# Optimization experiments

Measured on AMD Instinct MI355X. Metric: run time of the kernel, lower is better.

## Reference

```python
import jax, jax.numpy as jnp
import numpy as np

B, CH, CW, H, FH, FW = 32, 16, 16, 8, 4, 4
NQ = 64
NK = CH * FH * CW * FW  # 4096
D_IN, D_V, D_MODEL = 512, 64, 512


def setup_inputs() -> dict:
    key = jax.random.key(0)
    k1, k2, k3, k4, k5 = jax.random.split(key, 5)
    att12 = jax.random.uniform(k1, (B, CH, CW, H, FH, FW), dtype=jnp.float32)
    att3 = jax.random.uniform(k2, (B, H, NQ, CH * CW), dtype=jnp.float32)
    values = jax.random.normal(k3, (B, NK, D_IN), dtype=jnp.float32)
    # Learned params (xavier-ish scale)
    W_v = jax.random.normal(k4, (H * D_V, D_IN), dtype=jnp.float32) * (1.0 / np.sqrt(D_IN))
    b_v = jnp.zeros((H * D_V,), dtype=jnp.float32)
    W_o = jax.random.normal(k5, (D_MODEL, H * D_V), dtype=jnp.float32) * (1.0 / np.sqrt(H * D_V))
    b_o = jnp.zeros((D_MODEL,), dtype=jnp.float32)
    return {"att12": att12, "att3": att3, "values": values,
            "W_v": W_v, "b_v": b_v, "W_o": W_o, "b_o": b_o}


def reference(att12, att3, values, W_v, b_v, W_o, b_o):
    b_s, h, nq, _ = att3.shape
    ch = cw = CH
    fh, fw = att12.shape[-2:]
    nk = values.shape[1]
    d_v = W_v.shape[0] // h
    # v: [b, h, nk, d_v]
    v = (values @ W_v.T + b_v).reshape(b_s, nk, h, d_v).transpose(0, 2, 1, 3)
    # att12 -> [b, h, 1, ch, cw, fh, fw]
    a12 = jnp.transpose(att12, (0, 3, 1, 2, 4, 5))[:, :, None]
    # att3 -> [b, h, nq, ch, cw, 1, 1]
    a3 = att3.reshape(b_s, h, nq, ch, cw, 1, 1)
    # broadcast multiply, then interleave to key order (ch, fh, cw, fw)
    att = (a12 * a3).transpose(0, 1, 2, 3, 5, 4, 6).reshape(b_s, h, nq, nk)
    att = jax.nn.softmax(att, axis=-1)
    out = jnp.einsum('bhqk,bhkd->bhqd', att, v)
    out = out.transpose(0, 2, 1, 3).reshape(b_s, nq, h * d_v)
    return out @ W_o.T + b_o
```

## Files before the change

kernel.cpp:

```cpp
#include <hip/hip_runtime.h>
#include <stdint.h>

#define BB 32
#define HH 8
#define NQ 64
#define NK 4096
#define DIN 512
#define DV 64
#define DM 512

typedef short bf16x8 __attribute__((ext_vector_type(8)));
typedef short bf16x4 __attribute__((ext_vector_type(4)));
typedef float f32x4 __attribute__((ext_vector_type(4)));

__device__ __forceinline__ unsigned short f2bf(float f) {
  union { float f; unsigned u; } v; v.f = f;
  unsigned r = v.u + 0x7fffu + ((v.u >> 16) & 1u);
  return (unsigned short)(r >> 16);
}

__device__ __forceinline__ void gld_lds16(const void* g, void* l) {
  __builtin_amdgcn_global_load_lds(
      (const __attribute__((address_space(1))) void*)g,
      (__attribute__((address_space(3))) void*)l, 16, 0, 0);
}

__global__ __launch_bounds__(256) void convf2bf(const float* __restrict__ in,
                                                unsigned short* __restrict__ out) {
  long i = (long)(blockIdx.x * 256 + threadIdx.x) * 4;
  f32x4 d = *(const f32x4*)(in + i);
  bf16x4 o;
  o[0] = (short)f2bf(d[0]); o[1] = (short)f2bf(d[1]);
  o[2] = (short)f2bf(d[2]); o[3] = (short)f2bf(d[3]);
  *(bf16x4*)(out + i) = o;
}

__global__ __launch_bounds__(64) void zsum_kernel(const float* __restrict__ att12,
                                                  const float* __restrict__ att3,
                                                  float* __restrict__ rZ) {
  const int bhq = blockIdx.x;
  const int h = (bhq >> 6) & 7;
  const int b = bhq >> 9;
  const int l = threadIdx.x;
  const int ch = l >> 2, fh = l & 3;
  const float* a3p = att3 + (long)bhq * 256 + ch * 16;
  const float* a12p = att12 + (long)(b * 16 + ch) * 2048 + h * 16 + fh * 4;
  float sum = 0.f;
#pragma unroll
  for (int cw = 0; cw < 16; ++cw) {
    float y = a3p[cw];
    f32x4 x = *(const f32x4*)(a12p + cw * 128);
#pragma unroll
    for (int fw = 0; fw < 4; ++fw) sum += __expf(x[fw] * y);
  }
#pragma unroll
  for (int off = 32; off > 0; off >>= 1) sum += __shfl_down(sum, off);
  if (l == 0) rZ[bhq] = 1.0f / sum;
}

__global__ __launch_bounds__(256) void transpose_conv(const float* __restrict__ V,
                                                      unsigned short* __restrict__ Vt) {
  int id = blockIdx.x;
  int kt = id & 63;
  int ct = (id >> 6) & 7;
  int b = id >> 9;
  const int t = threadIdx.x;
  __shared__ __align__(16) unsigned short T[64][72];

  const float* vp = V + (long)b * (4096L * 512) + (long)(kt * 64) * 512 + ct * 64;
  int cc = (t & 15) * 4;
  int kk0 = t >> 4;
#pragma unroll
  for (int r = 0; r < 4; ++r) {
    int kk = kk0 + r * 16;
    f32x4 d = *(const f32x4*)(vp + (long)kk * 512 + cc);
    T[cc + 0][kk] = f2bf(d[0]);
    T[cc + 1][kk] = f2bf(d[1]);
    T[cc + 2][kk] = f2bf(d[2]);
    T[cc + 3][kk] = f2bf(d[3]);
  }
  __syncthreads();
  unsigned short* op = Vt + (long)b * (512L * 4096) + (long)(ct * 64) * 4096 + (long)(kt * 64);
#pragma unroll
  for (int s = 0; s < 2; ++s) {
    int li = s * 256 + t;
    int c = li >> 3, k8 = (li & 7) * 8;
    bf16x8 d = *(const bf16x8*)(&T[c][k8]);
    *(bf16x8*)(op + (long)c * 4096 + k8) = d;
  }
}

__global__ __launch_bounds__(256, 2) void fused_u_gemm(
    const float* __restrict__ att12, const float* __restrict__ att3,
    const float* __restrict__ rZ, const unsigned short* __restrict__ Vt,
    unsigned short* __restrict__ U) {
  const int id = blockIdx.x;
  const int xcd = id & 7, rest = id >> 3;
  const int m_t = rest & 3, bh = rest >> 2;
  const int b = bh * 2 + (xcd & 1);
  const int n_t = xcd >> 1;
  const int m0 = m_t * 128, n0 = n_t * 128;
  const int t = threadIdx.x, lane = t & 63, wave = t >> 6;

  const unsigned short* Vb = Vt + (long)b * (512L * 4096) + (long)n0 * 4096;
  __shared__ __align__(16) unsigned short As[128 * 32];
  __shared__ __align__(16) unsigned short Bs[128 * 32];

  const int r = t >> 1;
  const int kh = (t & 1) * 16;
  const int m = m0 + r, h = m >> 6, q = m & 63;
  const float* a3row = att3 + ((long)(b * 8 + h) * 64 + q) * 256;
  const float* a12bh = att12 + (long)b * 32768 + h * 16;

  const int wm = (wave >> 1) * 64, wn = (wave & 1) * 64;
  const int l16 = lane & 15, quad = lane >> 4;

  f32x4 acc[4][4];
#pragma unroll
  for (int i = 0; i < 4; ++i)
#pragma unroll
    for (int j = 0; j < 4; ++j) acc[i][j] = (f32x4){0.f, 0.f, 0.f, 0.f};

  for (int k0 = 0; k0 < 4096; k0 += 32) {
    {
      int row = t >> 2, kq = (t & 3) * 8;
      gld_lds16(Vb + (long)row * 4096 + k0 + kq, (char*)Bs + (wave * 64) * 16);
      int li = 256 + t;
      row = li >> 2; kq = (li & 3) * 8;
      gld_lds16(Vb + (long)row * 4096 + k0 + kq, (char*)Bs + (256 + wave * 64) * 16);
    }
    {
      int k = k0 + kh;
      int ch = k >> 8, fh = (k >> 6) & 3, cw0 = (k >> 2) & 15;
      f32x4 y = *(const f32x4*)(a3row + ch * 16 + cw0);
      const float* a12p = a12bh + (long)ch * 2048 + cw0 * 128 + fh * 4;
      bf16x8 p0, p1;
#pragma unroll
      for (int c4 = 0; c4 < 2; ++c4) {
        f32x4 x = *(const f32x4*)(a12p + c4 * 128);
#pragma unroll
        for (int fw = 0; fw < 4; ++fw) p0[c4 * 4 + fw] = (short)f2bf(__expf(x[fw] * y[c4]));
      }
#pragma unroll
      for (int c4 = 2; c4 < 4; ++c4) {
        f32x4 x = *(const f32x4*)(a12p + c4 * 128);
#pragma unroll
        for (int fw = 0; fw < 4; ++fw) p1[(c4 - 2) * 4 + fw] = (short)f2bf(__expf(x[fw] * y[c4]));
      }
      *(bf16x8*)(As + r * 32 + kh) = p0;
      *(bf16x8*)(As + r * 32 + kh + 8) = p1;
    }
    __syncthreads();
    bf16x8 af[4], bfr[4];
#pragma unroll
    for (int i = 0; i < 4; ++i)
      af[i] = *(const bf16x8*)(As + (wm + i * 16 + l16) * 32 + quad * 8);
#pragma unroll
    for (int j = 0; j < 4; ++j)
      bfr[j] = *(const bf16x8*)(Bs + (wn + j * 16 + l16) * 32 + quad * 8);
#pragma unroll
    for (int i = 0; i < 4; ++i)
#pragma unroll
      for (int j = 0; j < 4; ++j)
        acc[i][j] = __builtin_amdgcn_mfma_f32_16x16x32_bf16(af[i], bfr[j], acc[i][j], 0, 0, 0);
    __syncthreads();
  }

  const float* rzb = rZ + (long)b * 512;
  unsigned short* Ub = U + (long)b * 262144;
#pragma unroll
  for (int i = 0; i < 4; ++i) {
#pragma unroll
    for (int j = 0; j < 4; ++j) {
      int col = n0 + wn + j * 16 + l16;
#pragma unroll
      for (int rr = 0; rr < 4; ++rr) {
        int row = m0 + wm + i * 16 + quad * 4 + rr;
        float v = acc[i][j][rr] * rzb[row];
        Ub[(long)row * 512 + col] = f2bf(v);
      }
    }
  }
}

template <int BM, int BN, bool OUT_BF16, bool ADD_BIAS>
__global__ __launch_bounds__(256, 2) void gemm_bt(
    const unsigned short* __restrict__ A, const unsigned short* __restrict__ Bt,
    void* __restrict__ C, const float* __restrict__ bias,
    int K, int lda, int ldb, int ldc,
    long sA, long sB, int zmodB,
    long sC1, long sC2, int zdivC,
    long sBias, int zmodBias) {
  constexpr int BK = 32;
  const int t = threadIdx.x;
  const int lane = t & 63;
  const int wave = t >> 6;
  const int z = blockIdx.z;
  const int m0 = blockIdx.y * BM;
  const int n0 = blockIdx.x * BN;

  A += (long)z * sA + (long)m0 * lda;
  Bt += (long)(z % zmodB) * sB + (long)n0 * ldb;

  __shared__ __align__(16) unsigned short As[BM * BK];
  __shared__ __align__(16) unsigned short Bs[BN * BK];

  constexpr int TM = BM / 32;
  constexpr int TN = BN / 32;
  const int wm = (wave >> 1) * (BM / 2);
  const int wn = (wave & 1) * (BN / 2);
  const int l16 = lane & 15;
  const int quad = lane >> 4;

  f32x4 acc[TM][TN];
#pragma unroll
  for (int i = 0; i < TM; ++i)
#pragma unroll
    for (int j = 0; j < TN; ++j) acc[i][j] = (f32x4){0.f, 0.f, 0.f, 0.f};

  constexpr int ASHOT = (BM * 4) / 256;
  constexpr int BSHOT = (BN * 4) / 256;

  for (int k0 = 0; k0 < K; k0 += BK) {
#pragma unroll
    for (int s = 0; s < ASHOT; ++s) {
      int li = s * 256 + t;
      int row = li >> 2, kq = (li & 3) * 8;
      gld_lds16(A + (long)row * lda + k0 + kq, (char*)As + (s * 256 + wave * 64) * 16);
    }
#pragma unroll
    for (int s = 0; s < BSHOT; ++s) {
      int li = s * 256 + t;
      int row = li >> 2, kq = (li & 3) * 8;
      gld_lds16(Bt + (long)row * ldb + k0 + kq, (char*)Bs + (s * 256 + wave * 64) * 16);
    }
    __syncthreads();
    bf16x8 af[TM], bfr[TN];
#pragma unroll
    for (int i = 0; i < TM; ++i)
      af[i] = *(const bf16x8*)(As + (wm + i * 16 + l16) * BK + quad * 8);
#pragma unroll
    for (int j = 0; j < TN; ++j)
      bfr[j] = *(const bf16x8*)(Bs + (wn + j * 16 + l16) * BK + quad * 8);
#pragma unroll
    for (int i = 0; i < TM; ++i)
#pragma unroll
      for (int j = 0; j < TN; ++j)
        acc[i][j] = __builtin_amdgcn_mfma_f32_16x16x32_bf16(af[i], bfr[j], acc[i][j], 0, 0, 0);
    __syncthreads();
  }

  long coff = (long)(z / zdivC) * sC1 + (long)(z % zdivC) * sC2;
  const float* bp = nullptr;
  if (ADD_BIAS) bp = bias + (long)(z % zmodBias) * sBias + n0;
#pragma unroll
  for (int i = 0; i < TM; ++i) {
#pragma unroll
    for (int j = 0; j < TN; ++j) {
      int col = wn + j * 16 + l16;
#pragma unroll
      for (int r = 0; r < 4; ++r) {
        int row = wm + i * 16 + quad * 4 + r;
        float v = acc[i][j][r];
        if (ADD_BIAS) v += bp[col];
        long idx = coff + (long)(m0 + row) * ldc + (n0 + col);
        if (OUT_BF16) ((unsigned short*)C)[idx] = f2bf(v);
        else ((float*)C)[idx] = v;
      }
    }
  }
}

extern "C" void kernel_launch(void* const* d_in, const int* in_sizes, int n_in,
                              void* d_out, int out_size, void* d_ws, size_t ws_size,
                              hipStream_t stream) {
  const float* att12 = (const float*)d_in[0];
  const float* att3  = (const float*)d_in[1];
  const float* values = (const float*)d_in[2];
  const float* W_v = (const float*)d_in[3];
  const float* b_v = (const float*)d_in[4];
  const float* W_o = (const float*)d_in[5];
  const float* b_o = (const float*)d_in[6];
  float* out = (float*)d_out;

  char* ws = (char*)d_ws;
  unsigned short* Vt  = (unsigned short*)(ws);
  unsigned short* U   = (unsigned short*)(ws + 134217728L);
  unsigned short* Vo  = (unsigned short*)(ws + 150994944L);
  unsigned short* Wvb = (unsigned short*)(ws + 153092096L);
  unsigned short* Wob = (unsigned short*)(ws + 153616384L);
  float*          rZ  = (float*)(ws + 154140672L);

  convf2bf<<<dim3(256), dim3(256), 0, stream>>>(W_v, Wvb);
  convf2bf<<<dim3(256), dim3(256), 0, stream>>>(W_o, Wob);
  zsum_kernel<<<dim3(16384), dim3(64), 0, stream>>>(att12, att3, rZ);
  transpose_conv<<<dim3(16384), dim3(256), 0, stream>>>(values, Vt);

  fused_u_gemm<<<dim3(512), dim3(256), 0, stream>>>(att12, att3, rZ, Vt, U);

  gemm_bt<64, 64, true, true><<<dim3(1, 1, 256), dim3(256), 0, stream>>>(
      U, Wvb, Vo, b_v, 512, 512, 512, 512,
      32768L, 32768L, 8,
      32768L, 64L, 8,
      64L, 8);

  gemm_bt<128, 128, false, true><<<dim3(4, 16, 1), dim3(256), 0, stream>>>(
      Vo, Wob, out, b_o, 512, 512, 512, 512,
      0L, 0L, 1,
      0L, 0L, 1,
      0L, 1);

  (void)in_sizes; (void)n_in; (void)out_size; (void)ws_size;
}
```

Measured before the change: 608.7 us.

## Reorder computation: project values per head first, then attention, fuse softmax sum

Projects the values through W_v first, computing vT = W_v·V^T per batch with on-the-fly fp32→bf16 conversion. This replaces the separate transpose/convert pass and the old U=P·V GEMM over 512 input channels with a per-head P·v GEMM over 64 channels. The softmax denominator is now accumulated inside the attention GEMM across two K-splits, which removes the standalone zsum pass. Normalisation and b_v are applied while loading the output-projection operand, and the two K-split partials are summed through a duplicated W_o. The cost is more GEMM FLOPs in the projection, an fp32 intermediate, and a cross-wave LDS reduction.

After: 635.6 us. +4.4%, slower.

```diff
diff --git a/kernel.cpp b/kernel.cpp
--- a/kernel.cpp
+++ b/kernel.cpp
@@ -1,13 +1,4 @@
 #include <hip/hip_runtime.h>
-#include <stdint.h>
-
-#define BB 32
-#define HH 8
-#define NQ 64
-#define NK 4096
-#define DIN 512
-#define DV 64
-#define DM 512
 
 typedef short bf16x8 __attribute__((ext_vector_type(8)));
 typedef short bf16x4 __attribute__((ext_vector_type(4)));
@@ -25,8 +16,8 @@
       (__attribute__((address_space(3))) void*)l, 16, 0, 0);
 }
 
-__global__ __launch_bounds__(256) void convf2bf(const float* __restrict__ in,
-                                                unsigned short* __restrict__ out) {
+__global__ __launch_bounds__(256) void convWv(const float* __restrict__ in,
+                                              unsigned short* __restrict__ out) {
   long i = (long)(blockIdx.x * 256 + threadIdx.x) * 4;
   f32x4 d = *(const f32x4*)(in + i);
   bf16x4 o;
@@ -35,85 +26,33 @@
   *(bf16x4*)(out + i) = o;
 }
 
-__global__ __launch_bounds__(64) void zsum_kernel(const float* __restrict__ att12,
-                                                  const float* __restrict__ att3,
-                                                  float* __restrict__ rZ) {
-  const int bhq = blockIdx.x;
-  const int h = (bhq >> 6) & 7;
-  const int b = bhq >> 9;
-  const int l = threadIdx.x;
-  const int ch = l >> 2, fh = l & 3;
-  const float* a3p = att3 + (long)bhq * 256 + ch * 16;
-  const float* a12p = att12 + (long)(b * 16 + ch) * 2048 + h * 16 + fh * 4;
-  float sum = 0.f;
-#pragma unroll
-  for (int cw = 0; cw < 16; ++cw) {
-    float y = a3p[cw];
-    f32x4 x = *(const f32x4*)(a12p + cw * 128);
-#pragma unroll
-    for (int fw = 0; fw < 4; ++fw) sum += __expf(x[fw] * y);
-  }
-#pragma unroll
-  for (int off = 32; off > 0; off >>= 1) sum += __shfl_down(sum, off);
-  if (l == 0) rZ[bhq] = 1.0f / sum;
-}
-
-__global__ __launch_bounds__(256) void transpose_conv(const float* __restrict__ V,
-                                                      unsigned short* __restrict__ Vt) {
-  int id = blockIdx.x;
-  int kt = id & 63;
-  int ct = (id >> 6) & 7;
-  int b = id >> 9;
-  const int t = threadIdx.x;
-  __shared__ __align__(16) unsigned short T[64][72];
-
-  const float* vp = V + (long)b * (4096L * 512) + (long)(kt * 64) * 512 + ct * 64;
-  int cc = (t & 15) * 4;
-  int kk0 = t >> 4;
-#pragma unroll
-  for (int r = 0; r < 4; ++r) {
-    int kk = kk0 + r * 16;
-    f32x4 d = *(const f32x4*)(vp + (long)kk * 512 + cc);
-    T[cc + 0][kk] = f2bf(d[0]);
-    T[cc + 1][kk] = f2bf(d[1]);
-    T[cc + 2][kk] = f2bf(d[2]);
-    T[cc + 3][kk] = f2bf(d[3]);
-  }
-  __syncthreads();
-  unsigned short* op = Vt + (long)b * (512L * 4096) + (long)(ct * 64) * 4096 + (long)(kt * 64);
-#pragma unroll
-  for (int s = 0; s < 2; ++s) {
-    int li = s * 256 + t;
-    int c = li >> 3, k8 = (li & 7) * 8;
-    bf16x8 d = *(const bf16x8*)(&T[c][k8]);
-    *(bf16x8*)(op + (long)c * 4096 + k8) = d;
-  }
-}
-
-__global__ __launch_bounds__(256, 2) void fused_u_gemm(
-    const float* __restrict__ att12, const float* __restrict__ att3,
-    const float* __restrict__ rZ, const unsigned short* __restrict__ Vt,
-    unsigned short* __restrict__ U) {
-  const int id = blockIdx.x;
-  const int xcd = id & 7, rest = id >> 3;
-  const int m_t = rest & 3, bh = rest >> 2;
-  const int b = bh * 2 + (xcd & 1);
-  const int n_t = xcd >> 1;
-  const int m0 = m_t * 128, n0 = n_t * 128;
+__global__ __launch_bounds__(256) void convWo2(const float* __restrict__ in,
+                                               unsigned short* __restrict__ out) {
+  long i4 = (long)(blockIdx.x * 256 + threadIdx.x) * 4;
+  int e = (int)(i4 >> 9), c = (int)(i4 & 511);
+  f32x4 d = *(const f32x4*)(in + i4);
+  bf16x4 o;
+  o[0] = (short)f2bf(d[0]); o[1] = (short)f2bf(d[1]);
+  o[2] = (short)f2bf(d[2]); o[3] = (short)f2bf(d[3]);
+  *(bf16x4*)(out + (long)e * 1024 + c) = o;
+  *(bf16x4*)(out + (long)e * 1024 + 512 + c) = o;
+}
+
+__global__ __launch_bounds__(256, 2) void vt_gemm(
+    const unsigned short* __restrict__ Wvb, const float* __restrict__ V,
+    unsigned short* __restrict__ vT) {
   const int t = threadIdx.x, lane = t & 63, wave = t >> 6;
-
-  const unsigned short* Vb = Vt + (long)b * (512L * 4096) + (long)n0 * 4096;
-  __shared__ __align__(16) unsigned short As[128 * 32];
-  __shared__ __align__(16) unsigned short Bs[128 * 32];
-
-  const int r = t >> 1;
-  const int kh = (t & 1) * 16;
-  const int m = m0 + r, h = m >> 6, q = m & 63;
-  const float* a3row = att3 + ((long)(b * 8 + h) * 64 + q) * 256;
-  const float* a12bh = att12 + (long)b * 32768 + h * 16;
+  const int n0 = blockIdx.x * 128;
+  const int m0 = blockIdx.y * 128;
+  const int b = blockIdx.z;
+  const float* Vb = V + (long)b * (4096L * 512) + (long)n0 * 512;
+
+  __shared__ __align__(16) unsigned short As[128 * 64];
+  __shared__ __align__(16) unsigned short Bs[128 * 64];
 
   const int wm = (wave >> 1) * 64, wn = (wave & 1) * 64;
   const int l16 = lane & 15, quad = lane >> 4;
+  const int bchunk = (t & 15) * 4, brow0 = t >> 4;
 
   f32x4 acc[4][4];
 #pragma unroll
@@ -121,154 +60,236 @@
 #pragma unroll
     for (int j = 0; j < 4; ++j) acc[i][j] = (f32x4){0.f, 0.f, 0.f, 0.f};
 
-  for (int k0 = 0; k0 < 4096; k0 += 32) {
-    {
-      int row = t >> 2, kq = (t & 3) * 8;
-      gld_lds16(Vb + (long)row * 4096 + k0 + kq, (char*)Bs + (wave * 64) * 16);
-      int li = 256 + t;
-      row = li >> 2; kq = (li & 3) * 8;
-      gld_lds16(Vb + (long)row * 4096 + k0 + kq, (char*)Bs + (256 + wave * 64) * 16);
-    }
-    {
-      int k = k0 + kh;
-      int ch = k >> 8, fh = (k >> 6) & 3, cw0 = (k >> 2) & 15;
-      f32x4 y = *(const f32x4*)(a3row + ch * 16 + cw0);
-      const float* a12p = a12bh + (long)ch * 2048 + cw0 * 128 + fh * 4;
-      bf16x8 p0, p1;
-#pragma unroll
-      for (int c4 = 0; c4 < 2; ++c4) {
-        f32x4 x = *(const f32x4*)(a12p + c4 * 128);
-#pragma unroll
-        for (int fw = 0; fw < 4; ++fw) p0[c4 * 4 + fw] = (short)f2bf(__expf(x[fw] * y[c4]));
-      }
-#pragma unroll
-      for (int c4 = 2; c4 < 4; ++c4) {
-        f32x4 x = *(const f32x4*)(a12p + c4 * 128);
-#pragma unroll
-        for (int fw = 0; fw < 4; ++fw) p1[(c4 - 2) * 4 + fw] = (short)f2bf(__expf(x[fw] * y[c4]));
-      }
-      *(bf16x8*)(As + r * 32 + kh) = p0;
-      *(bf16x8*)(As + r * 32 + kh + 8) = p1;
-    }
-    __syncthreads();
-    bf16x8 af[4], bfr[4];
-#pragma unroll
-    for (int i = 0; i < 4; ++i)
-      af[i] = *(const bf16x8*)(As + (wm + i * 16 + l16) * 32 + quad * 8);
-#pragma unroll
-    for (int j = 0; j < 4; ++j)
-      bfr[j] = *(const bf16x8*)(Bs + (wn + j * 16 + l16) * 32 + quad * 8);
-#pragma unroll
-    for (int i = 0; i < 4; ++i)
+  for (int k0 = 0; k0 < 512; k0 += 64) {
+#pragma unroll
+    for (int s = 0; s < 4; ++s) {
+      int li = s * 256 + t;
+      int row = li >> 3, kq = (li & 7) * 8;
+      gld_lds16(Wvb + (long)(m0 + row) * 512 + k0 + kq, (char*)As + (s * 256 + wave * 64) * 16);
+    }
+#pragma unroll
+    for (int j = 0; j < 8; ++j) {
+      int row = brow0 + 16 * j;
+      f32x4 d = *(const f32x4*)(Vb + (long)row * 512 + k0 + bchunk);
+      bf16x4 p;
+      p[0] = (short)f2bf(d[0]); p[1] = (short)f2bf(d[1]);
+      p[2] = (short)f2bf(d[2]); p[3] = (short)f2bf(d[3]);
+      *(bf16x4*)(Bs + row * 64 + bchunk) = p;
+    }
+    __syncthreads();
+#pragma unroll
+    for (int ks = 0; ks < 2; ++ks) {
+      bf16x8 af[4], bfv[4];
+#pragma unroll
+      for (int i = 0; i < 4; ++i)
+        af[i] = *(const bf16x8*)(As + (wm + i * 16 + l16) * 64 + ks * 32 + quad * 8);
 #pragma unroll
       for (int j = 0; j < 4; ++j)
-        acc[i][j] = __builtin_amdgcn_mfma_f32_16x16x32_bf16(af[i], bfr[j], acc[i][j], 0, 0, 0);
-    __syncthreads();
-  }
-
-  const float* rzb = rZ + (long)b * 512;
-  unsigned short* Ub = U + (long)b * 262144;
-#pragma unroll
-  for (int i = 0; i < 4; ++i) {
+        bfv[j] = *(const bf16x8*)(Bs + (wn + j * 16 + l16) * 64 + ks * 32 + quad * 8);
+#pragma unroll
+      for (int i = 0; i < 4; ++i)
+#pragma unroll
+        for (int j = 0; j < 4; ++j)
+          acc[i][j] = __builtin_amdgcn_mfma_f32_16x16x32_bf16(af[i], bfv[j], acc[i][j], 0, 0, 0);
+    }
+    __syncthreads();
+  }
+  unsigned short* o = vT + (long)b * 2097152;
+#pragma unroll
+  for (int i = 0; i < 4; ++i)
 #pragma unroll
     for (int j = 0; j < 4; ++j) {
       int col = n0 + wn + j * 16 + l16;
 #pragma unroll
-      for (int rr = 0; rr < 4; ++rr) {
-        int row = m0 + wm + i * 16 + quad * 4 + rr;
-        float v = acc[i][j][rr] * rzb[row];
-        Ub[(long)row * 512 + col] = f2bf(v);
+      for (int r = 0; r < 4; ++r) {
+        int row = m0 + wm + i * 16 + quad * 4 + r;
+        o[(long)row * 4096 + col] = f2bf(acc[i][j][r]);
       }
     }
-  }
-}
-
-template <int BM, int BN, bool OUT_BF16, bool ADD_BIAS>
-__global__ __launch_bounds__(256, 2) void gemm_bt(
-    const unsigned short* __restrict__ A, const unsigned short* __restrict__ Bt,
-    void* __restrict__ C, const float* __restrict__ bias,
-    int K, int lda, int ldb, int ldc,
-    long sA, long sB, int zmodB,
-    long sC1, long sC2, int zdivC,
-    long sBias, int zmodBias) {
-  constexpr int BK = 32;
-  const int t = threadIdx.x;
-  const int lane = t & 63;
-  const int wave = t >> 6;
-  const int z = blockIdx.z;
-  const int m0 = blockIdx.y * BM;
-  const int n0 = blockIdx.x * BN;
-
-  A += (long)z * sA + (long)m0 * lda;
-  Bt += (long)(z % zmodB) * sB + (long)n0 * ldb;
-
-  __shared__ __align__(16) unsigned short As[BM * BK];
-  __shared__ __align__(16) unsigned short Bs[BN * BK];
-
-  constexpr int TM = BM / 32;
-  constexpr int TN = BN / 32;
-  const int wm = (wave >> 1) * (BM / 2);
-  const int wn = (wave & 1) * (BN / 2);
-  const int l16 = lane & 15;
-  const int quad = lane >> 4;
-
-  f32x4 acc[TM][TN];
-#pragma unroll
-  for (int i = 0; i < TM; ++i)
-#pragma unroll
-    for (int j = 0; j < TN; ++j) acc[i][j] = (f32x4){0.f, 0.f, 0.f, 0.f};
-
-  constexpr int ASHOT = (BM * 4) / 256;
-  constexpr int BSHOT = (BN * 4) / 256;
-
-  for (int k0 = 0; k0 < K; k0 += BK) {
-#pragma unroll
-    for (int s = 0; s < ASHOT; ++s) {
+}
+
+__global__ __launch_bounds__(256, 2) void o_gemm(
+    const float* __restrict__ att12, const float* __restrict__ att3,
+    const unsigned short* __restrict__ vT, float* __restrict__ O32,
+    float* __restrict__ Zp) {
+  const int bh = blockIdx.x, part = blockIdx.y;
+  const int b = bh >> 3, h = bh & 7;
+  const int t = threadIdx.x, lane = t & 63, wave = t >> 6;
+
+  __shared__ __align__(16) unsigned short As[4 * 64 * 32];
+  __shared__ __align__(16) unsigned short Bs[4 * 64 * 32];
+  __shared__ float Ored[64 * 64];
+  __shared__ float Zl[4][64];
+
+  const unsigned short* vTb = vT + (long)b * 2097152 + (long)h * 64 * 4096;
+  const int gq = t & 63, gw = t >> 6;
+  const float* a3row = att3 + ((long)bh * 64 + gq) * 256;
+  const float* a12b = att12 + (long)b * 32768 + h * 16;
+  const int l16 = lane & 15, quad = lane >> 4;
+  const int kw0 = part * 2048 + gw * 512;
+
+  f32x4 acc[4][4];
+#pragma unroll
+  for (int i = 0; i < 4; ++i)
+#pragma unroll
+    for (int j = 0; j < 4; ++j) acc[i][j] = (f32x4){0.f, 0.f, 0.f, 0.f};
+  float zacc = 0.f;
+
+  for (int it = 0; it < 16; ++it) {
+#pragma unroll
+    for (int s = 0; s < 4; ++s) {
+      int row = t >> 2, kq = (t & 3) * 8;
+      int kk = part * 2048 + s * 512 + it * 32 + kq;
+      gld_lds16(vTb + (long)row * 4096 + kk, (char*)Bs + s * 4096 + wave * 1024);
+    }
+    {
+      int kbase = kw0 + it * 32;
+      int ch = kbase >> 8, fh = (kbase >> 6) & 3, cw0 = (kbase >> 2) & 15;
+      f32x4 y0 = *(const f32x4*)(a3row + ch * 16 + cw0);
+      f32x4 y1 = *(const f32x4*)(a3row + ch * 16 + cw0 + 4);
+      const float* ap = a12b + ch * 2048 + cw0 * 128 + fh * 4;
+      bf16x8 p[4];
+#pragma unroll
+      for (int cw = 0; cw < 8; ++cw) {
+        float y = (cw < 4) ? y0[cw] : y1[cw - 4];
+        f32x4 x = *(const f32x4*)(ap + cw * 128);
+#pragma unroll
+        for (int fw = 0; fw < 4; ++fw) {
+          float e = __expf(x[fw] * y);
+          zacc += e;
+          p[cw >> 1][(cw & 1) * 4 + fw] = (short)f2bf(e);
+        }
+      }
+#pragma unroll
+      for (int g = 0; g < 4; ++g)
+        *(bf16x8*)(As + gw * 2048 + gq * 32 + g * 8) = p[g];
+    }
+    __syncthreads();
+    bf16x8 af[4], bfv[4];
+#pragma unroll
+    for (int i = 0; i < 4; ++i)
+      af[i] = *(const bf16x8*)(As + wave * 2048 + (i * 16 + l16) * 32 + quad * 8);
+#pragma unroll
+    for (int j = 0; j < 4; ++j)
+      bfv[j] = *(const bf16x8*)(Bs + wave * 2048 + (j * 16 + l16) * 32 + quad * 8);
+#pragma unroll
+    for (int i = 0; i < 4; ++i)
+#pragma unroll
+      for (int j = 0; j < 4; ++j)
+        acc[i][j] = __builtin_amdgcn_mfma_f32_16x16x32_bf16(af[i], bfv[j], acc[i][j], 0, 0, 0);
+    __syncthreads();
+  }
+
+  Zl[gw][gq] = zacc;
+#pragma unroll
+  for (int w = 0; w < 4; ++w) {
+    if (wave == w) {
+#pragma unroll
+      for (int i = 0; i < 4; ++i)
+#pragma unroll
+        for (int j = 0; j < 4; ++j) {
+          int col = j * 16 + l16;
+#pragma unroll
+          for (int r = 0; r < 4; ++r) {
+            int row = i * 16 + quad * 4 + r;
+            if (w == 0) Ored[row * 64 + col] = acc[i][j][r];
+            else Ored[row * 64 + col] += acc[i][j][r];
+          }
+        }
+    }
+    __syncthreads();
+  }
+  if (t < 64) {
+    float z = Zl[0][t] + Zl[1][t] + Zl[2][t] + Zl[3][t];
+    Zp[(long)part * 16384 + (long)bh * 64 + t] = z;
+  }
+  {
+    int q = t >> 2, c0 = (t & 3) * 16;
+    float* op = O32 + (long)part * 1048576 + ((long)(b * 64 + q)) * 512 + h * 64 + c0;
+#pragma unroll
+    for (int j = 0; j < 4; ++j)
+      *(f32x4*)(op + j * 4) = *(const f32x4*)(Ored + q * 64 + c0 + j * 4);
+  }
+}
+
+__global__ __launch_bounds__(256) void rzcomb(const float* __restrict__ Zp,
+                                              float* __restrict__ rZ) {
+  int i = blockIdx.x * 256 + threadIdx.x;
+  rZ[i] = 1.0f / (Zp[i] + Zp[16384 + i]);
+}
+
+__global__ __launch_bounds__(256, 2) void wo_gemm(
+    const float* __restrict__ O32, const float* __restrict__ rZ,
+    const float* __restrict__ b_v, const unsigned short* __restrict__ Wo2,
+    const float* __restrict__ b_o, float* __restrict__ out) {
+  const int t = threadIdx.x, lane = t & 63, wave = t >> 6;
+  const int n0 = blockIdx.x * 128;
+  const int m0 = blockIdx.y * 64;
+
+  __shared__ __align__(16) unsigned short As[64 * 32];
+  __shared__ __align__(16) unsigned short Bs[128 * 32];
+
+  const int wm = (wave >> 1) * 32, wn = (wave & 1) * 64;
+  const int l16 = lane & 15, quad = lane >> 4;
+  const int arow = t >> 2, akq = (t & 3) * 8;
+  const int m = m0 + arow, ab = m >> 6, aq = m & 63;
+
+  f32x4 acc[2][4];
+#pragma unroll
+  for (int i = 0; i < 2; ++i)
+#pragma unroll
+    for (int j = 0; j < 4; ++j) acc[i][j] = (f32x4){0.f, 0.f, 0.f, 0.f};
+
+  for (int k0 = 0; k0 < 1024; k0 += 32) {
+    int part = k0 >> 9, rem = k0 & 511;
+    int hh = (rem + akq) >> 6;
+    const float* src = O32 + (long)part * 1048576 + (long)m * 512 + rem + akq;
+    f32x4 x0 = *(const f32x4*)(src);
+    f32x4 x1 = *(const f32x4*)(src + 4);
+    float rz = rZ[ab * 512 + hh * 64 + aq];
+    f32x4 bv0 = (f32x4){0.f, 0.f, 0.f, 0.f}, bv1 = bv0;
+    if (part == 0) {
+      bv0 = *(const f32x4*)(b_v + rem + akq);
+      bv1 = *(const f32x4*)(b_v + rem + akq + 4);
+    }
+    bf16x8 pa;
+#pragma unroll
+    for (int j = 0; j < 4; ++j) pa[j] = (short)f2bf(x0[j] * rz + bv0[j]);
+#pragma unroll
+    for (int j = 0; j < 4; ++j) pa[4 + j] = (short)f2bf(x1[j] * rz + bv1[j]);
+    *(bf16x8*)(As + arow * 32 + akq) = pa;
+#pragma unroll
+    for (int s = 0; s < 2; ++s) {
       int li = s * 256 + t;
       int row = li >> 2, kq = (li & 3) * 8;
-      gld_lds16(A + (long)row * lda + k0 + kq, (char*)As + (s * 256 + wave * 64) * 16);
-    }
-#pragma unroll
-    for (int s = 0; s < BSHOT; ++s) {
-      int li = s * 256 + t;
-      int row = li >> 2, kq = (li & 3) * 8;
-      gld_lds16(Bt + (long)row * ldb + k0 + kq, (char*)Bs + (s * 256 + wave * 64) * 16);
-    }
-    __syncthreads();
-    bf16x8 af[TM], bfr[TN];
-#pragma unroll
-    for (int i = 0; i < TM; ++i)
-      af[i] = *(const bf16x8*)(As + (wm + i * 16 + l16) * BK + quad * 8);
-#pragma unroll
-    for (int j = 0; j < TN; ++j)
-      bfr[j] = *(const bf16x8*)(Bs + (wn + j * 16 + l16) * BK + quad * 8);
-#pragma unroll
-    for (int i = 0; i < TM; ++i)
-#pragma unroll
-      for (int j = 0; j < TN; ++j)
-        acc[i][j] = __builtin_amdgcn_mfma_f32_16x16x32_bf16(af[i], bfr[j], acc[i][j], 0, 0, 0);
-    __syncthreads();
-  }
-
-  long coff = (long)(z / zdivC) * sC1 + (long)(z % zdivC) * sC2;
-  const float* bp = nullptr;
-  if (ADD_BIAS) bp = bias + (long)(z % zmodBias) * sBias + n0;
-#pragma unroll
-  for (int i = 0; i < TM; ++i) {
-#pragma unroll
-    for (int j = 0; j < TN; ++j) {
-      int col = wn + j * 16 + l16;
+      gld_lds16(Wo2 + (long)(n0 + row) * 1024 + k0 + kq, (char*)Bs + (s * 256 + wave * 64) * 16);
+    }
+    __syncthreads();
+    bf16x8 af[2], bfv[4];
+#pragma unroll
+    for (int i = 0; i < 2; ++i)
+      af[i] = *(const bf16x8*)(As + (wm + i * 16 + l16) * 32 + quad * 8);
+#pragma unroll
+    for (int j = 0; j < 4; ++j)
+      bfv[j] = *(const bf16x8*)(Bs + (wn + j * 16 + l16) * 32 + quad * 8);
+#pragma unroll
+    for (int i = 0; i < 2; ++i)
+#pragma unroll
+      for (int j = 0; j < 4; ++j)
+        acc[i][j] = __builtin_amdgcn_mfma_f32_16x16x32_bf16(af[i], bfv[j], acc[i][j], 0, 0, 0);
+    __syncthreads();
+  }
+#pragma unroll
+  for (int i = 0; i < 2; ++i)
+#pragma unroll
+    for (int j = 0; j < 4; ++j) {
+      int col = n0 + wn + j * 16 + l16;
 #pragma unroll
       for (int r = 0; r < 4; ++r) {
         int row = wm + i * 16 + quad * 4 + r;
-        float v = acc[i][j][r];
-        if (ADD_BIAS) v += bp[col];
-        long idx = coff + (long)(m0 + row) * ldc + (n0 + col);
-        if (OUT_BF16) ((unsigned short*)C)[idx] = f2bf(v);
-        else ((float*)C)[idx] = v;
+        out[(long)(m0 + row) * 512 + col] = acc[i][j][r] + b_o[col];
       }
     }
-  }
 }
 
 extern "C" void kernel_launch(void* const* d_in, const int* in_sizes, int n_in,
@@ -284,31 +305,23 @@
   float* out = (float*)d_out;
 
   char* ws = (char*)d_ws;
-  unsigned short* Vt  = (unsigned short*)(ws);
-  unsigned short* U   = (unsigned short*)(ws + 134217728L);
-  unsigned short* Vo  = (unsigned short*)(ws + 150994944L);
-  unsigned short* Wvb = (unsigned short*)(ws + 153092096L);
-  unsigned short* Wob = (unsigned short*)(ws + 153616384L);
-  float*          rZ  = (float*)(ws + 154140672L);
-
-  convf2bf<<<dim3(256), dim3(256), 0, stream>>>(W_v, Wvb);
-  convf2bf<<<dim3(256), dim3(256), 0, stream>>>(W_o, Wob);
-  zsum_kernel<<<dim3(16384), dim3(64), 0, stream>>>(att12, att3, rZ);
-  transpose_conv<<<dim3(16384), dim3(256), 0, stream>>>(values, Vt);
-
-  fused_u_gemm<<<dim3(512), dim3(256), 0, stream>>>(att12, att3, rZ, Vt, U);
-
-  gemm_bt<64, 64, true, true><<<dim3(1, 1, 256), dim3(256), 0, stream>>>(
-      U, Wvb, Vo, b_v, 512, 512, 512, 512,
-      32768L, 32768L, 8,
-      32768L, 64L, 8,
-      64L, 8);
-
-  gemm_bt<128, 128, false, true><<<dim3(4, 16, 1), dim3(256), 0, stream>>>(
-      Vo, Wob, out, b_o, 512, 512, 512, 512,
-      0L, 0L, 1,
-      0L, 0L, 1,
-      0L, 1);
+  unsigned short* vT  = (unsigned short*)(ws);
+  float*          O32 = (float*)(ws + 134217728L);
+  float*          Zp  = (float*)(ws + 142606336L);
+  float*          rZ  = (float*)(ws + 142737408L);
+  unsigned short* Wvb = (unsigned short*)(ws + 142802944L);
+  unsigned short* Wo2 = (unsigned short*)(ws + 143327232L);
+
+  convWv<<<dim3(256), dim3(256), 0, stream>>>(W_v, Wvb);
+  convWo2<<<dim3(256), dim3(256), 0, stream>>>(W_o, Wo2);
+
+  vt_gemm<<<dim3(32, 4, 32), dim3(256), 0, stream>>>(Wvb, values, vT);
+
+  o_gemm<<<dim3(256, 2), dim3(256), 0, stream>>>(att12, att3, vT, O32, Zp);
+
+  rzcomb<<<dim3(64), dim3(256), 0, stream>>>(Zp, rZ);
+
+  wo_gemm<<<dim3(4, 32), dim3(256), 0, stream>>>(O32, rZ, b_v, Wo2, b_o, out);
 
   (void)in_sizes; (void)n_in; (void)out_size; (void)ws_size;
 }
```
